# Kernel tuning notes

Hardware: AMD Instinct MI355X
Metric: run time of the kernel (lower is better)

The kernel has to match this reference:

```python
import jax, jax.numpy as jnp
import numpy as np

N_NEWS, N_ENT, N_TOP = 100000, 50000, 2000
D = 128
N_EDGES = 1600000
HID, OUT = 512, 128


def setup_inputs() -> dict:
    key = jax.random.key(0)
    ks = jax.random.split(key, 12)
    return {
        "news_feats": jax.random.normal(ks[0], (N_NEWS, D), jnp.float32),
        "entity_feats": jax.random.normal(ks[1], (N_ENT, D), jnp.float32),
        "topic_feats": jax.random.normal(ks[2], (N_TOP, D), jnp.float32),
        "ent_row": jax.random.randint(ks[3], (N_EDGES,), 0, N_NEWS, jnp.int32),
        "ent_col": jax.random.randint(ks[4], (N_EDGES,), 0, N_ENT, jnp.int32),
        "top_row": jax.random.randint(ks[5], (N_EDGES,), 0, N_NEWS, jnp.int32),
        "top_col": jax.random.randint(ks[6], (N_EDGES,), 0, N_TOP, jnp.int32),
        "W1": jax.random.normal(ks[7], (3 * D, HID), jnp.float32) * 0.05,
        "b1": jnp.zeros((HID,), jnp.float32),
        "W2": jax.random.normal(ks[8], (HID, OUT), jnp.float32) * 0.05,
        "b2": jnp.zeros((OUT,), jnp.float32),
    }


def _agg(feats, row, col, num_news):
    # SpMM with binary adjacency: sum neighbor feats per news node
    gathered = feats[col]                                   # [E, D]
    summed = jax.ops.segment_sum(gathered, row, num_segments=num_news)
    deg = jax.ops.segment_sum(jnp.ones_like(row, dtype=feats.dtype), row,
                              num_segments=num_news)
    return summed / (deg[:, None] + 1e-8)


def reference(news_feats, entity_feats, topic_feats, ent_row, ent_col,
              top_row, top_col, W1, b1, W2, b2):
    n = news_feats.shape[0]
    ent_agg = _agg(entity_feats, ent_row, ent_col, n)
    top_agg = _agg(topic_feats, top_row, top_col, n)
    out = jnp.concatenate([news_feats, ent_agg, top_agg], axis=1)  # [N, 3D]
    h = jnp.tanh(out @ W1 + b1)
    return h @ W2 + b2
```

## Files before the change

### kernel.cpp

```cpp
#include <hip/hip_runtime.h>
#include <hip/hip_bf16.h>

#define NN 100000
#define NE 50000
#define NT 2000
#define DD 128
#define NEDGE 1600000
#define HID 512
#define OUTD 128
#define K1 (3*DD)
#define NBKT 391

typedef __bf16 bf16x8 __attribute__((ext_vector_type(8)));
typedef __bf16 bf16x4 __attribute__((ext_vector_type(4)));
typedef float  f32x4  __attribute__((ext_vector_type(4)));

__device__ __forceinline__ __bf16 f2b(float f) {
    __hip_bfloat16 h = __float2bfloat16(f);
    union { __hip_bfloat16 h; __bf16 b; } u; u.h = h; return u.b;
}

__device__ __forceinline__ void gll16(const void* g, void* l) {
    __builtin_amdgcn_global_load_lds((const __attribute__((address_space(1))) void*)g,
                                     (__attribute__((address_space(3))) void*)l, 16, 0, 0);
}

__device__ __forceinline__ float ftanh(float x) {
    x = fminf(fmaxf(x, -15.f), 15.f);
    float t = __expf(2.f * x);
    return (t - 1.f) / (t + 1.f);
}

__global__ void conv_feats(const float* __restrict__ entf, const float* __restrict__ topf,
                           const float* __restrict__ news,
                           __bf16* __restrict__ entb, __bf16* __restrict__ topb,
                           __bf16* __restrict__ X) {
    long i = ((long)blockIdx.x * 256 + threadIdx.x) * 4;
    const long NEL = (long)NE * DD;
    const long NTL = (long)NT * DD;
    if (i < NEL) {
        float4 v = *(const float4*)(entf + i);
        *(bf16x4*)(entb + i) = bf16x4{f2b(v.x), f2b(v.y), f2b(v.z), f2b(v.w)};
    } else if (i < NEL + NTL) {
        long j = i - NEL;
        float4 v = *(const float4*)(topf + j);
        *(bf16x4*)(topb + j) = bf16x4{f2b(v.x), f2b(v.y), f2b(v.z), f2b(v.w)};
    } else {
        long j = i - NEL - NTL;
        long row = j >> 7, col = j & 127;
        float4 v = *(const float4*)(news + j);
        *(bf16x4*)(X + row * K1 + col) = bf16x4{f2b(v.x), f2b(v.y), f2b(v.z), f2b(v.w)};
    }
}

__global__ __launch_bounds__(256) void hist_buckets(const int* __restrict__ er,
                                                    const int* __restrict__ tr,
                                                    int* __restrict__ bc_e,
                                                    int* __restrict__ bc_t) {
    __shared__ int lhe[NBKT], lht[NBKT];
    const int tid = threadIdx.x;
    for (int i = tid; i < NBKT; i += 256) { lhe[i] = 0; lht[i] = 0; }
    __syncthreads();
    const int base = blockIdx.x * 8192;
    #pragma unroll 4
    for (int k = 0; k < 32; k++) {
        int e = base + k * 256 + tid;
        if (e < NEDGE) {
            atomicAdd(&lhe[er[e] >> 8], 1);
            atomicAdd(&lht[tr[e] >> 8], 1);
        }
    }
    __syncthreads();
    for (int i = tid; i < NBKT; i += 256) {
        if (lhe[i]) atomicAdd(&bc_e[i], lhe[i]);
        if (lht[i]) atomicAdd(&bc_t[i], lht[i]);
    }
}

__global__ void scan_buckets(int* __restrict__ bc_e, int* __restrict__ bc_t,
                             int* __restrict__ cur_e, int* __restrict__ cur_t,
                             int* __restrict__ offs_e, int* __restrict__ offs_t) {
    int* bc  = blockIdx.y ? bc_t : bc_e;
    int* cur = blockIdx.y ? cur_t : cur_e;
    int* offs = blockIdx.y ? offs_t : offs_e;
    __shared__ int s[512];
    int i = threadIdx.x;
    s[i] = (i < NBKT) ? bc[i] : 0;
    __syncthreads();
    #pragma unroll
    for (int off = 1; off < 512; off <<= 1) {
        int v = (i >= off) ? s[i - off] : 0;
        __syncthreads();
        s[i] += v;
        __syncthreads();
    }
    if (i < NBKT) {
        bc[i] = s[i];
        cur[i] = i ? s[i - 1] : 0;
    }
    if (i == 0) offs[0] = 0;
}

__global__ __launch_bounds__(256) void scatter_bucket(const int* __restrict__ er,
                                                      const int* __restrict__ ec,
                                                      const int* __restrict__ tr,
                                                      const int* __restrict__ tc,
                                                      int* __restrict__ cur_e,
                                                      int* __restrict__ cur_t,
                                                      int* __restrict__ be,
                                                      int* __restrict__ bt) {
    __shared__ int lhe[NBKT], lht[NBKT];
    __shared__ int lbe[NBKT], lbt[NBKT];
    const int tid = threadIdx.x;
    for (int i = tid; i < NBKT; i += 256) { lhe[i] = 0; lht[i] = 0; }
    __syncthreads();
    const int base = blockIdx.x * 4096;
    #pragma unroll 4
    for (int k = 0; k < 16; k++) {
        int e = base + k * 256 + tid;
        if (e < NEDGE) {
            atomicAdd(&lhe[er[e] >> 8], 1);
            atomicAdd(&lht[tr[e] >> 8], 1);
        }
    }
    __syncthreads();
    for (int i = tid; i < NBKT; i += 256) {
        int c = lhe[i];
        lbe[i] = c ? atomicAdd(&cur_e[i], c) : 0;
        lhe[i] = 0;
        c = lht[i];
        lbt[i] = c ? atomicAdd(&cur_t[i], c) : 0;
        lht[i] = 0;
    }
    __syncthreads();
    #pragma unroll 4
    for (int k = 0; k < 16; k++) {
        int e = base + k * 256 + tid;
        if (e < NEDGE) {
            int r = er[e];
            int b = r >> 8;
            int p = lbe[b] + atomicAdd(&lhe[b], 1);
            be[p] = ((r & 255) << 16) | ec[e];
            r = tr[e];
            b = r >> 8;
            p = lbt[b] + atomicAdd(&lht[b], 1);
            bt[p] = ((r & 255) << 16) | tc[e];
        }
    }
}

__global__ __launch_bounds__(256) void bucket_csr(const int* __restrict__ be,
                                                  const int* __restrict__ bt,
                                                  const int* __restrict__ bc_e,
                                                  const int* __restrict__ bc_t,
                                                  int* __restrict__ offs_e,
                                                  int* __restrict__ offs_t,
                                                  int* __restrict__ se,
                                                  int* __restrict__ st) {
    const int* buf = blockIdx.y ? bt : be;
    const int* bc  = blockIdx.y ? bc_t : bc_e;
    int* offs      = blockIdx.y ? offs_t : offs_e;
    int* sout      = blockIdx.y ? st : se;
    const int b = blockIdx.x;
    const int tid = threadIdx.x;
    const int start = b ? bc[b - 1] : 0;
    const int cnt = bc[b] - start;

    __shared__ int scn[256];
    __shared__ int lcur[256];
    scn[tid] = 0;
    __syncthreads();
    for (int i = tid; i < cnt; i += 256)
        atomicAdd(&scn[buf[start + i] >> 16], 1);
    __syncthreads();
    #pragma unroll
    for (int off = 1; off < 256; off <<= 1) {
        int v = (tid >= off) ? scn[tid - off] : 0;
        __syncthreads();
        scn[tid] += v;
        __syncthreads();
    }
    const int node = b * 256 + tid;
    if (node < NN) offs[node + 1] = start + scn[tid];
    lcur[tid] = start + (tid ? scn[tid - 1] : 0);
    __syncthreads();
    for (int i = tid; i < cnt; i += 256) {
        int v = buf[start + i];
        int p = atomicAdd(&lcur[v >> 16], 1);
        sout[p] = v & 0xFFFF;
    }
}

__global__ __launch_bounds__(256) void aggregate2(const __bf16* __restrict__ entb,
                                                  const __bf16* __restrict__ topb,
                                                  const int* __restrict__ offs_e,
                                                  const int* __restrict__ offs_t,
                                                  const int* __restrict__ se,
                                                  const int* __restrict__ st,
                                                  __bf16* __restrict__ X) {
    const int wave = threadIdx.x >> 6, lane = threadIdx.x & 63;
    const int node = blockIdx.x * 4 + wave;
    if (node >= NN) return;
    const int h = lane >> 4;
    const int d = (lane & 15) * 8;

    float ea[8] = {0,0,0,0,0,0,0,0};
    float pa[8] = {0,0,0,0,0,0,0,0};

    const int s0 = offs_e[node], s1 = offs_e[node + 1];
    int i = s0 + h;
    for (; i + 12 < s1; i += 16) {
        int c0 = se[i], c1 = se[i + 4], c2 = se[i + 8], c3 = se[i + 12];
        bf16x8 v0 = *(const bf16x8*)(entb + (long)c0 * DD + d);
        bf16x8 v1 = *(const bf16x8*)(entb + (long)c1 * DD + d);
        bf16x8 v2 = *(const bf16x8*)(entb + (long)c2 * DD + d);
        bf16x8 v3 = *(const bf16x8*)(entb + (long)c3 * DD + d);
        #pragma unroll
        for (int j = 0; j < 8; j++)
            ea[j] += ((float)v0[j] + (float)v1[j]) + ((float)v2[j] + (float)v3[j]);
    }
    for (; i < s1; i += 4) {
        bf16x8 v = *(const bf16x8*)(entb + (long)se[i] * DD + d);
        #pragma unroll
        for (int j = 0; j < 8; j++) ea[j] += (float)v[j];
    }

    const int t0 = offs_t[node], t1 = offs_t[node + 1];
    i = t0 + h;
    for (; i + 12 < t1; i += 16) {
        int c0 = st[i], c1 = st[i + 4], c2 = st[i + 8], c3 = st[i + 12];
        bf16x8 v0 = *(const bf16x8*)(topb + (long)c0 * DD + d);
        bf16x8 v1 = *(const bf16x8*)(topb + (long)c1 * DD + d);
        bf16x8 v2 = *(const bf16x8*)(topb + (long)c2 * DD + d);
        bf16x8 v3 = *(const bf16x8*)(topb + (long)c3 * DD + d);
        #pragma unroll
        for (int j = 0; j < 8; j++)
            pa[j] += ((float)v0[j] + (float)v1[j]) + ((float)v2[j] + (float)v3[j]);
    }
    for (; i < t1; i += 4) {
        bf16x8 v = *(const bf16x8*)(topb + (long)st[i] * DD + d);
        #pragma unroll
        for (int j = 0; j < 8; j++) pa[j] += (float)v[j];
    }

    #pragma unroll
    for (int j = 0; j < 8; j++) {
        ea[j] += __shfl_xor(ea[j], 16, 64);
        ea[j] += __shfl_xor(ea[j], 32, 64);
        pa[j] += __shfl_xor(pa[j], 16, 64);
        pa[j] += __shfl_xor(pa[j], 32, 64);
    }

    const float ie = 1.0f / ((float)(s1 - s0) + 1e-8f);
    const float it = 1.0f / ((float)(t1 - t0) + 1e-8f);
    __bf16* xr = X + (long)node * K1;
    if (h == 1) {
        *(bf16x8*)(xr + DD + d) = bf16x8{f2b(ea[0]*ie), f2b(ea[1]*ie), f2b(ea[2]*ie), f2b(ea[3]*ie),
                                         f2b(ea[4]*ie), f2b(ea[5]*ie), f2b(ea[6]*ie), f2b(ea[7]*ie)};
    } else if (h == 2) {
        *(bf16x8*)(xr + 2*DD + d) = bf16x8{f2b(pa[0]*it), f2b(pa[1]*it), f2b(pa[2]*it), f2b(pa[3]*it),
                                           f2b(pa[4]*it), f2b(pa[5]*it), f2b(pa[6]*it), f2b(pa[7]*it)};
    }
}

__global__ void conv_w(const float* __restrict__ W1, const float* __restrict__ W2,
                       __bf16* __restrict__ W1T, __bf16* __restrict__ W2T) {
    int i = blockIdx.x * 256 + threadIdx.x;
    if (i < K1 * HID) {
        int k = i / HID, n = i % HID;
        W1T[n * K1 + k] = f2b(W1[i]);
    } else {
        int j = i - K1 * HID;
        if (j < HID * OUTD) {
            int k = j / OUTD, n = j % OUTD;
            W2T[n * HID + k] = f2b(W2[j]);
        }
    }
}


__device__ __forceinline__ void stage_tile(const __bf16* __restrict__ src, int ldK,
                                           int k0, int row0, int rowmax,
                                           __bf16* lds, int w, int lane) {
    #pragma unroll
    for (int half = 0; half < 2; half++) {
        int ss = w * 64 + half * 256 + lane;
        int r = ss >> 2;
        int sw = (r & 3) ^ ((r >> 2) & 3);
        int c = (ss & 3) ^ sw;
        int gr = row0 + r; if (gr >= rowmax) gr = rowmax - 1;
        gll16(src + (long)gr * ldK + k0 + c * 8,
              lds + (w * 64 + half * 256) * 8);
    }
}

__device__ __forceinline__ bf16x8 frag(const __bf16* lds, int r, int q) {
    int sw = (r & 3) ^ ((r >> 2) & 3);
    return *(const bf16x8*)(lds + (r * 4 + (q ^ sw)) * 8);
}

__device__ __forceinline__ void hs_write(__bf16* Hs, int r, int c, __bf16 v) {
    int ch = c >> 3;
    int pch = ((((ch >> 2) ^ ((r >> 2) & 3)) << 2) | ((ch & 3) ^ (r & 3)));
    Hs[(r * 16 + pch) * 8 + (c & 7)] = v;
}
__device__ __forceinline__ bf16x8 hs_frag(const __bf16* Hs, int r, int kk, int q) {
    int pch = (((kk ^ ((r >> 2) & 3)) << 2) | (q ^ (r & 3)));
    return *(const bf16x8*)(Hs + (r * 16 + pch) * 8);
}

__device__ __forceinline__ void stage_for_phase(int g, int bm,
        const __bf16* __restrict__ X, const __bf16* __restrict__ W1T,
        const __bf16* __restrict__ W2T,
        __bf16* Xs, __bf16* Wst, int w, int lane) {
    if (g >= 64) return;
    const int ncg = g >> 4, ph = g & 15;
    __bf16* wb = Wst + (g % 3) * 4096;
    if (ph < 12) {
        if (ncg == 0) stage_tile(X, K1, ph * 32, bm, NN, Xs + ph * 4096, w, lane);
        stage_tile(W1T, K1, ph * 32, ncg * 128, HID, wb, w, lane);
    } else {
        stage_tile(W2T, HID, ncg * 128 + (ph - 12) * 32, 0, OUTD, wb, w, lane);
    }
}

__global__ __launch_bounds__(256, 1) void mlp_fused(const __bf16* __restrict__ X,
                                                    const __bf16* __restrict__ W1T,
                                                    const float* __restrict__ b1,
                                                    const __bf16* __restrict__ W2T,
                                                    const float* __restrict__ b2,
                                                    float* __restrict__ out) {
    __shared__ __bf16 Xs[12 * 4096];
    __shared__ __bf16 Wst[3 * 4096];
    __shared__ __bf16 Hs[128 * 128];
    const int bm = blockIdx.x * 128;
    const int t = threadIdx.x;
    const int lane = t & 63;
    const int w = t >> 6;
    const int quad = lane >> 4;
    const int l16 = lane & 15;
    const int wm = w >> 1, wn = w & 1;

    float b1r[4][4], b2r[4];
    #pragma unroll
    for (int nc = 0; nc < 4; nc++)
        #pragma unroll
        for (int j = 0; j < 4; j++)
            b1r[nc][j] = b1[nc * 128 + wn * 64 + j * 16 + l16];
    #pragma unroll
    for (int j = 0; j < 4; j++) b2r[j] = b2[wn * 64 + j * 16 + l16];
    asm volatile("s_waitcnt vmcnt(0)" ::: "memory");

    f32x4 oacc[4][4];
    #pragma unroll
    for (int i = 0; i < 4; i++)
        #pragma unroll
        for (int j = 0; j < 4; j++)
            #pragma unroll
            for (int r = 0; r < 4; r++) oacc[i][j][r] = 0.0f;

    stage_for_phase(0, bm, X, W1T, W2T, Xs, Wst, w, lane);
    stage_for_phase(1, bm, X, W1T, W2T, Xs, Wst, w, lane);

    for (int nc = 0; nc < 4; nc++) {
        f32x4 hacc[4][4];
        #pragma unroll
        for (int i = 0; i < 4; i++)
            #pragma unroll
            for (int j = 0; j < 4; j++)
                #pragma unroll
                for (int r = 0; r < 4; r++) hacc[i][j][r] = 0.0f;

        #pragma unroll
        for (int kt = 0; kt < 12; kt++) {
            if (nc == 0 && kt <= 10) asm volatile("s_waitcnt vmcnt(4)" ::: "memory");
            else                     asm volatile("s_waitcnt vmcnt(2)" ::: "memory");
            __builtin_amdgcn_s_barrier();
            const __bf16* xb = Xs + kt * 4096;
            const __bf16* wb = Wst + ((nc * 16 + kt) % 3) * 4096;
            bf16x8 af[4], bfr[4];
            #pragma unroll
            for (int i = 0; i < 4; i++) {
                af[i]  = frag(xb, wm * 64 + i * 16 + l16, quad);
                bfr[i] = frag(wb, wn * 64 + i * 16 + l16, quad);
            }
            stage_for_phase(nc * 16 + kt + 2, bm, X, W1T, W2T, Xs, Wst, w, lane);
            __builtin_amdgcn_s_setprio(1);
            #pragma unroll
            for (int i = 0; i < 4; i++)
                #pragma unroll
                for (int j = 0; j < 4; j++)
                    hacc[i][j] = __builtin_amdgcn_mfma_f32_16x16x32_bf16(af[i], bfr[j], hacc[i][j], 0, 0, 0);
            __builtin_amdgcn_s_setprio(0);
        }

        #pragma unroll
        for (int j = 0; j < 4; j++) {
            const int col = wn * 64 + j * 16 + l16;
            const float bb = b1r[nc][j];
            #pragma unroll
            for (int i = 0; i < 4; i++) {
                const int rbase = wm * 64 + i * 16 + quad * 4;
                #pragma unroll
                for (int r = 0; r < 4; r++)
                    hs_write(Hs, rbase + r, col, f2b(ftanh(hacc[i][j][r] + bb)));
            }
        }
        asm volatile("s_waitcnt lgkmcnt(0)" ::: "memory");
        __builtin_amdgcn_s_barrier();

        #pragma unroll
        for (int kk = 0; kk < 4; kk++) {
            if (nc == 3 && kk == 3) asm volatile("s_waitcnt vmcnt(0)" ::: "memory");
            else                    asm volatile("s_waitcnt vmcnt(2)" ::: "memory");
            __builtin_amdgcn_s_barrier();
            const __bf16* wb = Wst + ((nc * 16 + 12 + kk) % 3) * 4096;
            bf16x8 af[4], bfr[4];
            #pragma unroll
            for (int i = 0; i < 4; i++) {
                af[i]  = hs_frag(Hs, wm * 64 + i * 16 + l16, kk, quad);
                bfr[i] = frag(wb, wn * 64 + i * 16 + l16, quad);
            }
            stage_for_phase(nc * 16 + 12 + kk + 2, bm, X, W1T, W2T, Xs, Wst, w, lane);
            __builtin_amdgcn_s_setprio(1);
            #pragma unroll
            for (int i = 0; i < 4; i++)
                #pragma unroll
                for (int j = 0; j < 4; j++)
                    oacc[i][j] = __builtin_amdgcn_mfma_f32_16x16x32_bf16(af[i], bfr[j], oacc[i][j], 0, 0, 0);
            __builtin_amdgcn_s_setprio(0);
        }
    }

    #pragma unroll
    for (int i = 0; i < 4; i++) {
        #pragma unroll
        for (int r = 0; r < 4; r++) {
            const int gr = bm + wm * 64 + i * 16 + quad * 4 + r;
            if (gr < NN) {
                float* orow = out + (long)gr * OUTD + wn * 64 + l16;
                #pragma unroll
                for (int j = 0; j < 4; j++)
                    orow[j * 16] = oacc[i][j][r] + b2r[j];
            }
        }
    }
}

extern "C" void kernel_launch(void* const* d_in, const int* in_sizes, int n_in,
                              void* d_out, int out_size, void* d_ws, size_t ws_size,
                              hipStream_t stream) {
    const float* news  = (const float*)d_in[0];
    const float* ent_f = (const float*)d_in[1];
    const float* top_f = (const float*)d_in[2];
    const int* ent_row = (const int*)d_in[3];
    const int* ent_col = (const int*)d_in[4];
    const int* top_row = (const int*)d_in[5];
    const int* top_col = (const int*)d_in[6];
    const float* W1 = (const float*)d_in[7];
    const float* b1 = (const float*)d_in[8];
    const float* W2 = (const float*)d_in[9];
    const float* b2 = (const float*)d_in[10];

    char* ws = (char*)d_ws;
    int* offs_e = (int*)(ws + 0);
    int* offs_t = (int*)(ws + 400016);
    int* bc_e   = (int*)(ws + 800032);
    int* bc_t   = (int*)(ws + 801596);
    int* cur_e  = (int*)(ws + 803160);
    int* cur_t  = (int*)(ws + 804724);
    int* be     = (int*)(ws + 806320);
    int* bt     = (int*)(ws + 7206320);
    int* se     = (int*)(ws + 13606320);
    int* st     = (int*)(ws + 20006320);
    __bf16* entb = (__bf16*)(ws + 26406336);
    __bf16* topb = (__bf16*)(ws + 39206336);
    __bf16* X   = (__bf16*)(ws + 102400000);
    __bf16* W1T = (__bf16*)(ws + 179200000);
    __bf16* W2T = (__bf16*)(ws + 179593216);

    hipMemsetAsync(ws + 800032, 0, 6256, stream);
    conv_w<<<1024, 256, 0, stream>>>(W1, W2, W1T, W2T);
    conv_feats<<<19000, 256, 0, stream>>>(ent_f, top_f, news, entb, topb, X);
    hist_buckets<<<196, 256, 0, stream>>>(ent_row, top_row, bc_e, bc_t);
    scan_buckets<<<dim3(1, 2), 512, 0, stream>>>(bc_e, bc_t, cur_e, cur_t, offs_e, offs_t);
    scatter_bucket<<<392, 256, 0, stream>>>(ent_row, ent_col, top_row, top_col,
                                            cur_e, cur_t, be, bt);
    bucket_csr<<<dim3(NBKT, 2), 256, 0, stream>>>(be, bt, bc_e, bc_t,
                                                  offs_e, offs_t, se, st);
    aggregate2<<<NN / 4, 256, 0, stream>>>(entb, topb, offs_e, offs_t, se, st, X);
    mlp_fused<<<782, 256, 0, stream>>>(X, W1T, b1, W2T, b2, (float*)d_out);
}
```

Measured before the change: 536.0 us.

## Restructure fused MLP to 512 threads with 64-wide K stages and split H buffer

Rewrites the fused two-layer MLP kernel to use 8 waves per block (2x4 wave grid) and stage K in 64-element chunks, so there are half as many barrier phases. The hidden tile is now written in two 64-column halves into a smaller LDS buffer, which lets half the waves do their tanh writes while the second GEMM consumes the first half. Staging and fragment offsets are precomputed once, and the waitcnt and barrier are fused into single asm sequences. The aim is more latency hiding and fewer synchronisations per tile, at the cost of higher LDS use and more complex cross-wave ordering.

```diff
diff --git a/kernel.cpp b/kernel.cpp
--- a/kernel.cpp
+++ b/kernel.cpp
@@ -30,6 +30,12 @@
     float t = __expf(2.f * x);
     return (t - 1.f) / (t + 1.f);
 }
+
+__device__ __forceinline__ void sync_v4() { asm volatile("s_waitcnt vmcnt(4)\n\ts_barrier" ::: "memory"); }
+__device__ __forceinline__ void sync_v2() { asm volatile("s_waitcnt vmcnt(2)\n\ts_barrier" ::: "memory"); }
+__device__ __forceinline__ void sync_lgkm_v2() { asm volatile("s_waitcnt lgkmcnt(0) vmcnt(2)\n\ts_barrier" ::: "memory"); }
+__device__ __forceinline__ void sync_lgkm_v0() { asm volatile("s_waitcnt lgkmcnt(0) vmcnt(0)\n\ts_barrier" ::: "memory"); }
+__device__ __forceinline__ void bar_only() { asm volatile("s_barrier" ::: "memory"); }
 
 __global__ void conv_feats(const float* __restrict__ entf, const float* __restrict__ topf,
                            const float* __restrict__ news,
@@ -279,155 +285,222 @@
 }
 
 
-__device__ __forceinline__ void stage_tile(const __bf16* __restrict__ src, int ldK,
-                                           int k0, int row0, int rowmax,
-                                           __bf16* lds, int w, int lane) {
-    #pragma unroll
-    for (int half = 0; half < 2; half++) {
-        int ss = w * 64 + half * 256 + lane;
-        int r = ss >> 2;
-        int sw = (r & 3) ^ ((r >> 2) & 3);
-        int c = (ss & 3) ^ sw;
-        int gr = row0 + r; if (gr >= rowmax) gr = rowmax - 1;
-        gll16(src + (long)gr * ldK + k0 + c * 8,
-              lds + (w * 64 + half * 256) * 8);
-    }
-}
-
-__device__ __forceinline__ bf16x8 frag(const __bf16* lds, int r, int q) {
-    int sw = (r & 3) ^ ((r >> 2) & 3);
-    return *(const bf16x8*)(lds + (r * 4 + (q ^ sw)) * 8);
-}
-
-__device__ __forceinline__ void hs_write(__bf16* Hs, int r, int c, __bf16 v) {
-    int ch = c >> 3;
-    int pch = ((((ch >> 2) ^ ((r >> 2) & 3)) << 2) | ((ch & 3) ^ (r & 3)));
-    Hs[(r * 16 + pch) * 8 + (c & 7)] = v;
-}
-__device__ __forceinline__ bf16x8 hs_frag(const __bf16* Hs, int r, int kk, int q) {
-    int pch = (((kk ^ ((r >> 2) & 3)) << 2) | (q ^ (r & 3)));
-    return *(const bf16x8*)(Hs + (r * 16 + pch) * 8);
-}
-
-__device__ __forceinline__ void stage_for_phase(int g, int bm,
-        const __bf16* __restrict__ X, const __bf16* __restrict__ W1T,
-        const __bf16* __restrict__ W2T,
-        __bf16* Xs, __bf16* Wst, int w, int lane) {
-    if (g >= 64) return;
-    const int ncg = g >> 4, ph = g & 15;
-    __bf16* wb = Wst + (g % 3) * 4096;
-    if (ph < 12) {
-        if (ncg == 0) stage_tile(X, K1, ph * 32, bm, NN, Xs + ph * 4096, w, lane);
-        stage_tile(W1T, K1, ph * 32, ncg * 128, HID, wb, w, lane);
-    } else {
-        stage_tile(W2T, HID, ncg * 128 + (ph - 12) * 32, 0, OUTD, wb, w, lane);
-    }
-}
-
-__global__ __launch_bounds__(256, 1) void mlp_fused(const __bf16* __restrict__ X,
+__global__ __launch_bounds__(512, 1) void mlp_fused(const __bf16* __restrict__ X,
                                                     const __bf16* __restrict__ W1T,
                                                     const float* __restrict__ b1,
                                                     const __bf16* __restrict__ W2T,
                                                     const float* __restrict__ b2,
                                                     float* __restrict__ out) {
     __shared__ __bf16 Xs[12 * 4096];
-    __shared__ __bf16 Wst[3 * 4096];
-    __shared__ __bf16 Hs[128 * 128];
+    __shared__ __bf16 Wst[6 * 4096];
+    __shared__ __bf16 HsH[128 * 64];
     const int bm = blockIdx.x * 128;
     const int t = threadIdx.x;
     const int lane = t & 63;
     const int w = t >> 6;
     const int quad = lane >> 4;
     const int l16 = lane & 15;
-    const int wm = w >> 1, wn = w & 1;
-
-    float b1r[4][4], b2r[4];
+    const int wm = w >> 2, wn = w & 3;
+
+    const int r_st = t >> 2;
+    const int sw_st = (r_st & 3) ^ ((r_st >> 2) & 3);
+    const int c_st = (t & 3) ^ sw_st;
+    int grx = bm + r_st; if (grx >= NN) grx = NN - 1;
+    const long xoff  = (long)grx * K1 + c_st * 8;
+    const long w1off = (long)r_st * K1 + c_st * 8;
+    const long w2off = (long)r_st * HID + c_st * 8;
+    int aoff[4], boff[2], hoff[4][2];
+    #pragma unroll
+    for (int i = 0; i < 4; i++) {
+        const int r = wm * 64 + i * 16 + l16;
+        const int sw = (r & 3) ^ ((r >> 2) & 3);
+        aoff[i] = (r * 4 + (quad ^ sw)) * 8;
+        const int p0 = quad ^ (r & 3);
+        const int bb = (r >> 2) & 1;
+        hoff[i][0] = (r * 8 + (p0 | ((0 ^ bb) << 2))) * 8;
+        hoff[i][1] = (r * 8 + (p0 | ((1 ^ bb) << 2))) * 8;
+    }
+    #pragma unroll
+    for (int j = 0; j < 2; j++) {
+        const int r = wn * 32 + j * 16 + l16;
+        const int sw = (r & 3) ^ ((r >> 2) & 3);
+        boff[j] = (r * 4 + (quad ^ sw)) * 8;
+    }
+
+    float b1r[4][2], b2r[2];
     #pragma unroll
     for (int nc = 0; nc < 4; nc++)
         #pragma unroll
-        for (int j = 0; j < 4; j++)
-            b1r[nc][j] = b1[nc * 128 + wn * 64 + j * 16 + l16];
-    #pragma unroll
-    for (int j = 0; j < 4; j++) b2r[j] = b2[wn * 64 + j * 16 + l16];
+        for (int j = 0; j < 2; j++)
+            b1r[nc][j] = b1[nc * 128 + wn * 32 + j * 16 + l16];
+    #pragma unroll
+    for (int j = 0; j < 2; j++) b2r[j] = b2[wn * 32 + j * 16 + l16];
     asm volatile("s_waitcnt vmcnt(0)" ::: "memory");
 
-    f32x4 oacc[4][4];
+    f32x4 oacc[4][2];
     #pragma unroll
     for (int i = 0; i < 4; i++)
         #pragma unroll
-        for (int j = 0; j < 4; j++)
+        for (int j = 0; j < 2; j++)
             #pragma unroll
             for (int r = 0; r < 4; r++) oacc[i][j][r] = 0.0f;
 
-    stage_for_phase(0, bm, X, W1T, W2T, Xs, Wst, w, lane);
-    stage_for_phase(1, bm, X, W1T, W2T, Xs, Wst, w, lane);
-
+    auto stage_group = [&](int g) {
+        if (g >= 32) return;
+        const int gn = g >> 3, gp = g & 7;
+        __bf16* slot = Wst + (g % 3) * 8192;
+        if (gp < 6) {
+            const int k0 = gp * 64;
+            if (gn == 0) {
+                __bf16* xu = Xs + gp * 8192;
+                gll16(X + xoff + k0,      xu + t * 8);
+                gll16(X + xoff + k0 + 32, xu + 4096 + t * 8);
+            }
+            const long wo = w1off + (long)gn * 128 * K1 + k0;
+            gll16(W1T + wo,      slot + t * 8);
+            gll16(W1T + wo + 32, slot + 4096 + t * 8);
+        } else {
+            const long wo = w2off + gn * 128 + (gp - 6) * 64;
+            gll16(W2T + wo,      slot + t * 8);
+            gll16(W2T + wo + 32, slot + 4096 + t * 8);
+        }
+    };
+
+    stage_group(0);
+    stage_group(1);
+
+    #pragma unroll
     for (int nc = 0; nc < 4; nc++) {
-        f32x4 hacc[4][4];
+        f32x4 hacc[4][2];
         #pragma unroll
         for (int i = 0; i < 4; i++)
             #pragma unroll
-            for (int j = 0; j < 4; j++)
+            for (int j = 0; j < 2; j++)
                 #pragma unroll
                 for (int r = 0; r < 4; r++) hacc[i][j][r] = 0.0f;
 
         #pragma unroll
-        for (int kt = 0; kt < 12; kt++) {
-            if (nc == 0 && kt <= 10) asm volatile("s_waitcnt vmcnt(4)" ::: "memory");
-            else                     asm volatile("s_waitcnt vmcnt(2)" ::: "memory");
-            __builtin_amdgcn_s_barrier();
-            const __bf16* xb = Xs + kt * 4096;
-            const __bf16* wb = Wst + ((nc * 16 + kt) % 3) * 4096;
-            bf16x8 af[4], bfr[4];
+        for (int kt = 0; kt < 6; kt++) {
+            const int p = nc * 8 + kt;
+            if (p < 5) sync_v4(); else sync_v2();
+            const __bf16* xu = Xs + kt * 8192;
+            const __bf16* slot = Wst + (p % 3) * 8192;
+            bf16x8 a0[4], a1[4], bw0[2], bw1[2];
             #pragma unroll
             for (int i = 0; i < 4; i++) {
-                af[i]  = frag(xb, wm * 64 + i * 16 + l16, quad);
-                bfr[i] = frag(wb, wn * 64 + i * 16 + l16, quad);
-            }
-            stage_for_phase(nc * 16 + kt + 2, bm, X, W1T, W2T, Xs, Wst, w, lane);
+                a0[i] = *(const bf16x8*)(xu + aoff[i]);
+                a1[i] = *(const bf16x8*)(xu + 4096 + aoff[i]);
+            }
+            #pragma unroll
+            for (int j = 0; j < 2; j++) {
+                bw0[j] = *(const bf16x8*)(slot + boff[j]);
+                bw1[j] = *(const bf16x8*)(slot + 4096 + boff[j]);
+            }
+            stage_group(p + 2);
             __builtin_amdgcn_s_setprio(1);
             #pragma unroll
             for (int i = 0; i < 4; i++)
                 #pragma unroll
-                for (int j = 0; j < 4; j++)
-                    hacc[i][j] = __builtin_amdgcn_mfma_f32_16x16x32_bf16(af[i], bfr[j], hacc[i][j], 0, 0, 0);
+                for (int j = 0; j < 2; j++)
+                    hacc[i][j] = __builtin_amdgcn_mfma_f32_16x16x32_bf16(a0[i], bw0[j], hacc[i][j], 0, 0, 0);
+            #pragma unroll
+            for (int i = 0; i < 4; i++)
+                #pragma unroll
+                for (int j = 0; j < 2; j++)
+                    hacc[i][j] = __builtin_amdgcn_mfma_f32_16x16x32_bf16(a1[i], bw1[j], hacc[i][j], 0, 0, 0);
             __builtin_amdgcn_s_setprio(0);
         }
 
-        #pragma unroll
-        for (int j = 0; j < 4; j++) {
-            const int col = wn * 64 + j * 16 + l16;
-            const float bb = b1r[nc][j];
+        if (wn < 2) {
+            #pragma unroll
+            for (int j = 0; j < 2; j++) {
+                const int cl = wn * 32 + j * 16 + l16;
+                const int ch = cl >> 3;
+                const float bb = b1r[nc][j];
+                #pragma unroll
+                for (int i = 0; i < 4; i++) {
+                    const int rb = wm * 64 + i * 16 + quad * 4;
+                    #pragma unroll
+                    for (int r = 0; r < 4; r++) {
+                        const int rr = rb + r;
+                        const int pch = ((ch & 3) ^ (rr & 3)) | ((((ch >> 2) ^ (rr >> 2)) & 1) << 2);
+                        HsH[(rr * 8 + pch) * 8 + (cl & 7)] = f2b(ftanh(hacc[i][j][r] + bb));
+                    }
+                }
+            }
+        }
+        sync_lgkm_v2();
+
+        {
+            const int p = nc * 8 + 6;
+            const __bf16* slot = Wst + (p % 3) * 8192;
+            bf16x8 ah[4][2], bh[2][2];
             #pragma unroll
             for (int i = 0; i < 4; i++) {
-                const int rbase = wm * 64 + i * 16 + quad * 4;
-                #pragma unroll
-                for (int r = 0; r < 4; r++)
-                    hs_write(Hs, rbase + r, col, f2b(ftanh(hacc[i][j][r] + bb)));
-            }
-        }
-        asm volatile("s_waitcnt lgkmcnt(0)" ::: "memory");
-        __builtin_amdgcn_s_barrier();
-
-        #pragma unroll
-        for (int kk = 0; kk < 4; kk++) {
-            if (nc == 3 && kk == 3) asm volatile("s_waitcnt vmcnt(0)" ::: "memory");
-            else                    asm volatile("s_waitcnt vmcnt(2)" ::: "memory");
-            __builtin_amdgcn_s_barrier();
-            const __bf16* wb = Wst + ((nc * 16 + 12 + kk) % 3) * 4096;
-            bf16x8 af[4], bfr[4];
+                ah[i][0] = *(const bf16x8*)(HsH + hoff[i][0]);
+                ah[i][1] = *(const bf16x8*)(HsH + hoff[i][1]);
+            }
+            #pragma unroll
+            for (int j = 0; j < 2; j++) {
+                bh[j][0] = *(const bf16x8*)(slot + boff[j]);
+                bh[j][1] = *(const bf16x8*)(slot + 4096 + boff[j]);
+            }
+            stage_group(p + 2);
+            __builtin_amdgcn_s_setprio(1);
+            #pragma unroll
+            for (int u = 0; u < 2; u++)
+                #pragma unroll
+                for (int i = 0; i < 4; i++)
+                    #pragma unroll
+                    for (int j = 0; j < 2; j++)
+                        oacc[i][j] = __builtin_amdgcn_mfma_f32_16x16x32_bf16(ah[i][u], bh[j][u], oacc[i][j], 0, 0, 0);
+            __builtin_amdgcn_s_setprio(0);
+        }
+        bar_only();
+
+        if (wn >= 2) {
+            #pragma unroll
+            for (int j = 0; j < 2; j++) {
+                const int cl = (wn - 2) * 32 + j * 16 + l16;
+                const int ch = cl >> 3;
+                const float bb = b1r[nc][j];
+                #pragma unroll
+                for (int i = 0; i < 4; i++) {
+                    const int rb = wm * 64 + i * 16 + quad * 4;
+                    #pragma unroll
+                    for (int r = 0; r < 4; r++) {
+                        const int rr = rb + r;
+                        const int pch = ((ch & 3) ^ (rr & 3)) | ((((ch >> 2) ^ (rr >> 2)) & 1) << 2);
+                        HsH[(rr * 8 + pch) * 8 + (cl & 7)] = f2b(ftanh(hacc[i][j][r] + bb));
+                    }
+                }
+            }
+        }
+        if (nc == 3) sync_lgkm_v0(); else sync_lgkm_v2();
+
+        {
+            const int p = nc * 8 + 7;
+            const __bf16* slot = Wst + (p % 3) * 8192;
+            bf16x8 ah[4][2], bh[2][2];
             #pragma unroll
             for (int i = 0; i < 4; i++) {
-                af[i]  = hs_frag(Hs, wm * 64 + i * 16 + l16, kk, quad);
-                bfr[i] = frag(wb, wn * 64 + i * 16 + l16, quad);
-            }
-            stage_for_phase(nc * 16 + 12 + kk + 2, bm, X, W1T, W2T, Xs, Wst, w, lane);
+                ah[i][0] = *(const bf16x8*)(HsH + hoff[i][0]);
+                ah[i][1] = *(const bf16x8*)(HsH + hoff[i][1]);
+            }
+            #pragma unroll
+            for (int j = 0; j < 2; j++) {
+                bh[j][0] = *(const bf16x8*)(slot + boff[j]);
+                bh[j][1] = *(const bf16x8*)(slot + 4096 + boff[j]);
+            }
+            stage_group(p + 2);
             __builtin_amdgcn_s_setprio(1);
             #pragma unroll
-            for (int i = 0; i < 4; i++)
-                #pragma unroll
-                for (int j = 0; j < 4; j++)
-                    oacc[i][j] = __builtin_amdgcn_mfma_f32_16x16x32_bf16(af[i], bfr[j], oacc[i][j], 0, 0, 0);
+            for (int u = 0; u < 2; u++)
+                #pragma unroll
+                for (int i = 0; i < 4; i++)
+                    #pragma unroll
+                    for (int j = 0; j < 2; j++)
+                        oacc[i][j] = __builtin_amdgcn_mfma_f32_16x16x32_bf16(ah[i][u], bh[j][u], oacc[i][j], 0, 0, 0);
             __builtin_amdgcn_s_setprio(0);
         }
     }
@@ -438,10 +511,9 @@
         for (int r = 0; r < 4; r++) {
             const int gr = bm + wm * 64 + i * 16 + quad * 4 + r;
             if (gr < NN) {
-                float* orow = out + (long)gr * OUTD + wn * 64 + l16;
-                #pragma unroll
-                for (int j = 0; j < 4; j++)
-                    orow[j * 16] = oacc[i][j][r] + b2r[j];
+                float* orow = out + (long)gr * OUTD + wn * 32 + l16;
+                orow[0]  = oacc[i][0][r] + b2r[0];
+                orow[16] = oacc[i][1][r] + b2r[1];
             }
         }
     }
@@ -489,5 +561,5 @@
     bucket_csr<<<dim3(NBKT, 2), 256, 0, stream>>>(be, bt, bc_e, bc_t,
                                                   offs_e, offs_t, se, st);
     aggregate2<<<NN / 4, 256, 0, stream>>>(entb, topb, offs_e, offs_t, se, st, X);
-    mlp_fused<<<782, 256, 0, stream>>>(X, W1T, b1, W2T, b2, (float*)d_out);
-}
+    mlp_fused<<<782, 512, 0, stream>>>(X, W1T, b1, W2T, b2, (float*)d_out);
+}
```

Measured after the change: 538.3 us. No clear change (+0.4%).

## Restructure fused MLP to 64-row tiles with all hidden chunks in registers

Applied to the files above, without the earlier changes.

The fused MLP kernel now processes 64 rows per block instead of 128 and keeps accumulators for all four hidden chunks live at once. Each X k-slice is loaded once and reused across the whole hidden width, using a 3-deep X ring and a double-buffered W1 stage. The W1 staging LDS is then reused for the tanh output and a 3-slot W2 ring. Grid size doubles and LDS use drops, which is meant to improve occupancy and load balance across CUs. The cost is more register pressure and W1/W2 being re-read by twice as many blocks.

```diff
diff --git a/kernel.cpp b/kernel.cpp
--- a/kernel.cpp
+++ b/kernel.cpp
@@ -30,6 +30,8 @@
     float t = __expf(2.f * x);
     return (t - 1.f) / (t + 1.f);
 }
+
+__device__ __forceinline__ void bar_only() { asm volatile("s_barrier" ::: "memory"); }
 
 __global__ void conv_feats(const float* __restrict__ entf, const float* __restrict__ topf,
                            const float* __restrict__ news,
@@ -309,31 +311,15 @@
     return *(const bf16x8*)(Hs + (r * 16 + pch) * 8);
 }
 
-__device__ __forceinline__ void stage_for_phase(int g, int bm,
-        const __bf16* __restrict__ X, const __bf16* __restrict__ W1T,
-        const __bf16* __restrict__ W2T,
-        __bf16* Xs, __bf16* Wst, int w, int lane) {
-    if (g >= 64) return;
-    const int ncg = g >> 4, ph = g & 15;
-    __bf16* wb = Wst + (g % 3) * 4096;
-    if (ph < 12) {
-        if (ncg == 0) stage_tile(X, K1, ph * 32, bm, NN, Xs + ph * 4096, w, lane);
-        stage_tile(W1T, K1, ph * 32, ncg * 128, HID, wb, w, lane);
-    } else {
-        stage_tile(W2T, HID, ncg * 128 + (ph - 12) * 32, 0, OUTD, wb, w, lane);
-    }
-}
-
-__global__ __launch_bounds__(256, 1) void mlp_fused(const __bf16* __restrict__ X,
-                                                    const __bf16* __restrict__ W1T,
-                                                    const float* __restrict__ b1,
-                                                    const __bf16* __restrict__ W2T,
-                                                    const float* __restrict__ b2,
-                                                    float* __restrict__ out) {
-    __shared__ __bf16 Xs[12 * 4096];
-    __shared__ __bf16 Wst[3 * 4096];
-    __shared__ __bf16 Hs[128 * 128];
-    const int bm = blockIdx.x * 128;
+__global__ __launch_bounds__(256) void mlp_fused(const __bf16* __restrict__ X,
+                                                 const __bf16* __restrict__ W1T,
+                                                 const float* __restrict__ b1,
+                                                 const __bf16* __restrict__ W2T,
+                                                 const float* __restrict__ b2,
+                                                 float* __restrict__ out) {
+    __shared__ __bf16 Xs[3][2048];
+    __shared__ __bf16 Wreg[8][4096];
+    const int bm = blockIdx.x * 64;
     const int t = threadIdx.x;
     const int lane = t & 63;
     const int w = t >> 6;
@@ -341,6 +327,25 @@
     const int l16 = lane & 15;
     const int wm = w >> 1, wn = w & 1;
 
+    const int r_sx = t >> 2;
+    const int sw_sx = (r_sx & 3) ^ ((r_sx >> 2) & 3);
+    const int c_sx = (t & 3) ^ sw_sx;
+    int grx = bm + r_sx; if (grx >= NN) grx = NN - 1;
+    const long xsrc = (long)grx * K1 + c_sx * 8;
+    int aoff[2], boff[4];
+    #pragma unroll
+    for (int i = 0; i < 2; i++) {
+        const int r = wm * 32 + i * 16 + l16;
+        const int sw = (r & 3) ^ ((r >> 2) & 3);
+        aoff[i] = (r * 4 + (quad ^ sw)) * 8;
+    }
+    #pragma unroll
+    for (int j = 0; j < 4; j++) {
+        const int r = wn * 64 + j * 16 + l16;
+        const int sw = (r & 3) ^ ((r >> 2) & 3);
+        boff[j] = (r * 4 + (quad ^ sw)) * 8;
+    }
+
     float b1r[4][4], b2r[4];
     #pragma unroll
     for (int nc = 0; nc < 4; nc++)
@@ -351,92 +356,126 @@
     for (int j = 0; j < 4; j++) b2r[j] = b2[wn * 64 + j * 16 + l16];
     asm volatile("s_waitcnt vmcnt(0)" ::: "memory");
 
-    f32x4 oacc[4][4];
-    #pragma unroll
-    for (int i = 0; i < 4; i++)
-        #pragma unroll
-        for (int j = 0; j < 4; j++)
-            #pragma unroll
-            for (int r = 0; r < 4; r++) oacc[i][j][r] = 0.0f;
-
-    stage_for_phase(0, bm, X, W1T, W2T, Xs, Wst, w, lane);
-    stage_for_phase(1, bm, X, W1T, W2T, Xs, Wst, w, lane);
-
-    for (int nc = 0; nc < 4; nc++) {
-        f32x4 hacc[4][4];
-        #pragma unroll
-        for (int i = 0; i < 4; i++)
+    f32x4 hacc[4][2][4];
+    #pragma unroll
+    for (int nc = 0; nc < 4; nc++)
+        #pragma unroll
+        for (int i = 0; i < 2; i++)
             #pragma unroll
             for (int j = 0; j < 4; j++)
                 #pragma unroll
-                for (int r = 0; r < 4; r++) hacc[i][j][r] = 0.0f;
-
-        #pragma unroll
-        for (int kt = 0; kt < 12; kt++) {
-            if (nc == 0 && kt <= 10) asm volatile("s_waitcnt vmcnt(4)" ::: "memory");
-            else                     asm volatile("s_waitcnt vmcnt(2)" ::: "memory");
-            __builtin_amdgcn_s_barrier();
-            const __bf16* xb = Xs + kt * 4096;
-            const __bf16* wb = Wst + ((nc * 16 + kt) % 3) * 4096;
-            bf16x8 af[4], bfr[4];
-            #pragma unroll
-            for (int i = 0; i < 4; i++) {
-                af[i]  = frag(xb, wm * 64 + i * 16 + l16, quad);
-                bfr[i] = frag(wb, wn * 64 + i * 16 + l16, quad);
-            }
-            stage_for_phase(nc * 16 + kt + 2, bm, X, W1T, W2T, Xs, Wst, w, lane);
-            __builtin_amdgcn_s_setprio(1);
-            #pragma unroll
-            for (int i = 0; i < 4; i++)
+                for (int r = 0; r < 4; r++) hacc[nc][i][j][r] = 0.0f;
+
+    gll16(X + xsrc, &Xs[0][0] + t * 8);
+    #pragma unroll
+    for (int nc = 0; nc < 4; nc++)
+        stage_tile(W1T, K1, 0, nc * 128, HID, &Wreg[nc][0], w, lane);
+    gll16(X + xsrc + 32, &Xs[1][0] + t * 8);
+
+    #pragma unroll
+    for (int kt = 0; kt < 12; kt++) {
+        if (kt < 11) asm volatile("s_waitcnt vmcnt(1)\n\ts_barrier" ::: "memory");
+        else         asm volatile("s_waitcnt vmcnt(0)\n\ts_barrier" ::: "memory");
+        const __bf16* xb = &Xs[kt % 3][0];
+        const __bf16* wb = &Wreg[(kt & 1) * 4][0];
+        bf16x8 a0 = *(const bf16x8*)(xb + aoff[0]);
+        bf16x8 a1 = *(const bf16x8*)(xb + aoff[1]);
+        if (kt < 11) {
+            __bf16* wnx = &Wreg[((kt + 1) & 1) * 4][0];
+            #pragma unroll
+            for (int nc = 0; nc < 4; nc++)
+                stage_tile(W1T, K1, (kt + 1) * 32, nc * 128, HID, wnx + nc * 4096, w, lane);
+        }
+        if (kt < 10)
+            gll16(X + xsrc + (kt + 2) * 32, &Xs[(kt + 2) % 3][0] + t * 8);
+        __builtin_amdgcn_s_setprio(1);
+        #pragma unroll
+        for (int nc = 0; nc < 4; nc++) {
+            bf16x8 bw[4];
+            #pragma unroll
+            for (int j = 0; j < 4; j++)
+                bw[j] = *(const bf16x8*)(wb + nc * 4096 + boff[j]);
+            #pragma unroll
+            for (int i = 0; i < 2; i++) {
+                bf16x8 av = i ? a1 : a0;
                 #pragma unroll
                 for (int j = 0; j < 4; j++)
-                    hacc[i][j] = __builtin_amdgcn_mfma_f32_16x16x32_bf16(af[i], bfr[j], hacc[i][j], 0, 0, 0);
-            __builtin_amdgcn_s_setprio(0);
-        }
-
+                    hacc[nc][i][j] = __builtin_amdgcn_mfma_f32_16x16x32_bf16(av, bw[j], hacc[nc][i][j], 0, 0, 0);
+            }
+        }
+        __builtin_amdgcn_s_setprio(0);
+    }
+
+    f32x4 oacc[2][4];
+    #pragma unroll
+    for (int i = 0; i < 2; i++)
+        #pragma unroll
+        for (int j = 0; j < 4; j++)
+            #pragma unroll
+            for (int r = 0; r < 4; r++) oacc[i][j][r] = 0.0f;
+
+    __bf16* Hs = &Wreg[0][0];
+    bar_only();
+
+    auto stage_w2 = [&](int g) {
+        const int ncg = g >> 1, half = g & 1, s = g % 3;
+        stage_tile(W2T, HID, ncg * 128 + half * 64,      0, OUTD, &Wreg[2 + 2 * s][0], w, lane);
+        stage_tile(W2T, HID, ncg * 128 + half * 64 + 32, 0, OUTD, &Wreg[3 + 2 * s][0], w, lane);
+    };
+    stage_w2(0);
+    stage_w2(1);
+
+    #pragma unroll
+    for (int nc = 0; nc < 4; nc++) {
+        if (nc > 0) bar_only();
         #pragma unroll
         for (int j = 0; j < 4; j++) {
-            const int col = wn * 64 + j * 16 + l16;
+            const int cl = wn * 64 + j * 16 + l16;
             const float bb = b1r[nc][j];
             #pragma unroll
-            for (int i = 0; i < 4; i++) {
-                const int rbase = wm * 64 + i * 16 + quad * 4;
+            for (int i = 0; i < 2; i++) {
+                const int rb = wm * 32 + i * 16 + quad * 4;
                 #pragma unroll
                 for (int r = 0; r < 4; r++)
-                    hs_write(Hs, rbase + r, col, f2b(ftanh(hacc[i][j][r] + bb)));
+                    hs_write(Hs, rb + r, cl, f2b(ftanh(hacc[nc][i][j][r] + bb)));
             }
         }
-        asm volatile("s_waitcnt lgkmcnt(0)" ::: "memory");
-        __builtin_amdgcn_s_barrier();
-
-        #pragma unroll
-        for (int kk = 0; kk < 4; kk++) {
-            if (nc == 3 && kk == 3) asm volatile("s_waitcnt vmcnt(0)" ::: "memory");
-            else                    asm volatile("s_waitcnt vmcnt(2)" ::: "memory");
-            __builtin_amdgcn_s_barrier();
-            const __bf16* wb = Wst + ((nc * 16 + 12 + kk) % 3) * 4096;
-            bf16x8 af[4], bfr[4];
-            #pragma unroll
-            for (int i = 0; i < 4; i++) {
-                af[i]  = hs_frag(Hs, wm * 64 + i * 16 + l16, kk, quad);
-                bfr[i] = frag(wb, wn * 64 + i * 16 + l16, quad);
+        #pragma unroll
+        for (int p2 = 0; p2 < 2; p2++) {
+            const int q = nc * 2 + p2;
+            if (q < 7) asm volatile("s_waitcnt lgkmcnt(0) vmcnt(4)\n\ts_barrier" ::: "memory");
+            else       asm volatile("s_waitcnt lgkmcnt(0) vmcnt(0)\n\ts_barrier" ::: "memory");
+            const __bf16* s0 = &Wreg[2 + 2 * (q % 3)][0];
+            bf16x8 ah[2][2], bh[4][2];
+            #pragma unroll
+            for (int i = 0; i < 2; i++) {
+                const int rr = wm * 32 + i * 16 + l16;
+                ah[i][0] = hs_frag(Hs, rr, p2 * 2 + 0, quad);
+                ah[i][1] = hs_frag(Hs, rr, p2 * 2 + 1, quad);
             }
-            stage_for_phase(nc * 16 + 12 + kk + 2, bm, X, W1T, W2T, Xs, Wst, w, lane);
+            #pragma unroll
+            for (int j = 0; j < 4; j++) {
+                bh[j][0] = *(const bf16x8*)(s0 + boff[j]);
+                bh[j][1] = *(const bf16x8*)(s0 + 4096 + boff[j]);
+            }
+            if (q < 6) stage_w2(q + 2);
             __builtin_amdgcn_s_setprio(1);
             #pragma unroll
-            for (int i = 0; i < 4; i++)
+            for (int u = 0; u < 2; u++)
                 #pragma unroll
-                for (int j = 0; j < 4; j++)
-                    oacc[i][j] = __builtin_amdgcn_mfma_f32_16x16x32_bf16(af[i], bfr[j], oacc[i][j], 0, 0, 0);
+                for (int i = 0; i < 2; i++)
+                    #pragma unroll
+                    for (int j = 0; j < 4; j++)
+                        oacc[i][j] = __builtin_amdgcn_mfma_f32_16x16x32_bf16(ah[i][u], bh[j][u], oacc[i][j], 0, 0, 0);
             __builtin_amdgcn_s_setprio(0);
         }
     }
 
     #pragma unroll
-    for (int i = 0; i < 4; i++) {
+    for (int i = 0; i < 2; i++) {
         #pragma unroll
         for (int r = 0; r < 4; r++) {
-            const int gr = bm + wm * 64 + i * 16 + quad * 4 + r;
+            const int gr = bm + wm * 32 + i * 16 + quad * 4 + r;
             if (gr < NN) {
                 float* orow = out + (long)gr * OUTD + wn * 64 + l16;
                 #pragma unroll
@@ -489,5 +528,5 @@
     bucket_csr<<<dim3(NBKT, 2), 256, 0, stream>>>(be, bt, bc_e, bc_t,
                                                   offs_e, offs_t, se, st);
     aggregate2<<<NN / 4, 256, 0, stream>>>(entb, topb, offs_e, offs_t, se, st, X);
-    mlp_fused<<<782, 256, 0, stream>>>(X, W1T, b1, W2T, b2, (float*)d_out);
-}
+    mlp_fused<<<1563, 256, 0, stream>>>(X, W1T, b1, W2T, b2, (float*)d_out);
+}
```

New measurement: 527.1 us. Within noise of the previous version (-1.7%).
